# Kernel optimization log

Measured on AMD Instinct MI355X. Metric: run time of the kernel, lower is better.

Reference implementation:

```python
import jax, jax.numpy as jnp
import numpy as np

C = 256
G = 32            # GroupNorm groups = min(32, C)
DQK = C // 8      # q/k channel dim
EPS = 1e-5


def setup_inputs() -> dict:
    key = jax.random.key(0)
    ks = jax.random.split(key, 10)
    B, H, W = 4, 64, 64
    s = 0.02
    return {
        "x": jax.random.normal(ks[0], (B, C, H, W), dtype=jnp.float32),
        "gamma": jnp.ones((C,), jnp.float32),
        "beta": jnp.zeros((C,), jnp.float32),
        "wq": jax.random.normal(ks[1], (DQK, C), jnp.float32) * s,
        "bq": jnp.zeros((DQK,), jnp.float32),
        "wk": jax.random.normal(ks[2], (DQK, C), jnp.float32) * s,
        "bk": jnp.zeros((DQK,), jnp.float32),
        "wv": jax.random.normal(ks[3], (C, C), jnp.float32) * s,
        "bv": jnp.zeros((C,), jnp.float32),
        "wp": jax.random.normal(ks[4], (C, C), jnp.float32) * s,
        "bp": jnpp if False else jnp.zeros((C,), jnp.float32),
    }


def reference(x, gamma, beta, wq, bq, wk, bk, wv, bv, wp, bp):
    B, Cc, H, W = x.shape
    N = H * W
    # GroupNorm(32, C), affine
    h = x.reshape(B, G, Cc // G, H, W)
    mu = h.mean(axis=(2, 3, 4), keepdims=True)
    var = h.var(axis=(2, 3, 4), keepdims=True)
    h = (h - mu) * jax.lax.rsqrt(var + EPS)
    h = h.reshape(B, Cc, N) * gamma[:, None] + beta[:, None]
    # 1x1 convs == per-token linear maps over channels
    q = jnp.einsum('dc,bcn->bnd', wq, h) + bq            # [B, N, DQK]
    k = jnp.einsum('dc,bcn->bdn', wk, h) + bk[:, None]   # [B, DQK, N]
    v = jnp.einsum('ec,bcn->ben', wv, h) + bv[:, None]   # [B, C, N]
    scale = DQK ** (-0.5)
    attn = jax.nn.softmax(jnp.einsum('bnd,bdm->bnm', q, k) * scale, axis=-1)
    out = jnp.einsum('bnm,bem->ben', attn, v)            # [B, C, N]
    proj = jnp.einsum('fe,ben->bfn', wp, out) + bp[:, None]
    return x + proj.reshape(B, Cc, H, W)
```

## Files before the change

kernel.cpp:

```cpp
#include <hip/hip_runtime.h>
#include <hip/hip_bf16.h>

#define NB 4
#define CD 256
#define NT 4096
#define DQ 32

typedef __attribute__((ext_vector_type(8))) __bf16 bf16x8;
typedef __attribute__((ext_vector_type(16))) float float16v;
typedef __attribute__((ext_vector_type(4))) unsigned int uint4v;
typedef __attribute__((ext_vector_type(2))) unsigned int uint2v;

#if __has_builtin(__builtin_amdgcn_exp2f)
#define EXP2(x) __builtin_amdgcn_exp2f(x)
#else
#define EXP2(x) exp2f(x)
#endif

__device__ inline unsigned short f2bf(float f) {
  unsigned u = __float_as_uint(f);
  u += 0x7fffu + ((u >> 16) & 1u);
  return (unsigned short)(u >> 16);
}

#define BARRIER() asm volatile("s_waitcnt lgkmcnt(0)\n\ts_barrier" ::: "memory")

__global__ __launch_bounds__(1024) void stats_pack(
    const float* __restrict__ x, const float* __restrict__ gamma,
    const float* __restrict__ beta, const float* __restrict__ wq,
    const float* __restrict__ wk, const float* __restrict__ wv,
    const float* __restrict__ wp, const float* __restrict__ bq,
    const float* __restrict__ bk, const float* __restrict__ bv,
    float* __restrict__ sc, float* __restrict__ sh,
    unsigned short* __restrict__ wqkv, unsigned short* __restrict__ wpb,
    float* __restrict__ bias) {
  int bx = blockIdx.x;
  int tid = threadIdx.x;
  if (bx < 128) {
    int b = bx >> 5, g = bx & 31;
    const float4* xp = (const float4*)(x + (size_t)bx * 32768);
    float s = 0.f, ss = 0.f;
#pragma unroll
    for (int i = 0; i < 8; i++) {
      float4 t4 = xp[i * 1024 + tid];
      s += t4.x + t4.y + t4.z + t4.w;
      ss += t4.x * t4.x + t4.y * t4.y + t4.z * t4.z + t4.w * t4.w;
    }
#pragma unroll
    for (int off = 32; off >= 1; off >>= 1) {
      s += __shfl_xor(s, off);
      ss += __shfl_xor(ss, off);
    }
    __shared__ float red[32];
    int wid = tid >> 6;
    if ((tid & 63) == 0) {
      red[wid] = s;
      red[16 + wid] = ss;
    }
    __syncthreads();
    if (tid < 8) {
      float S = 0.f, SS = 0.f;
#pragma unroll
      for (int i = 0; i < 16; i++) {
        S += red[i];
        SS += red[16 + i];
      }
      float mu = S * (1.f / 32768.f);
      float rstd = rsqrtf(SS * (1.f / 32768.f) - mu * mu + 1e-5f);
      int c = g * 8 + tid;
      float gm = gamma[c];
      sc[b * CD + c] = gm * rstd;
      sh[b * CD + c] = beta[c] - mu * gm * rstd;
    }
  } else {
    const float scale2 = 0.2550348909867343f;
    int i = (bx - 128) * 1024 + tid;
    if (i < 320 * 256) {
      int j = i >> 8, c = i & 255;
      float v;
      if (j < 32) v = wq[j * 256 + c] * scale2;
      else if (j < 64) v = wk[(j - 32) * 256 + c];
      else v = wv[(j - 64) * 256 + c];
      wqkv[i] = f2bf(v);
    } else if (i < 320 * 256 + 256 * 256) {
      int k = i - 320 * 256;
      wpb[k] = f2bf(wp[k]);
    } else if (i < 320 * 256 + 256 * 256 + 320) {
      int j = i - (320 * 256 + 256 * 256);
      float v;
      if (j < 32) v = bq[j] * scale2;
      else if (j < 64) v = bk[j - 32];
      else v = bv[j - 64];
      bias[j] = v;
    }
  }
}

__global__ __launch_bounds__(512) void qkv_norm(
    const float* __restrict__ x, const float* __restrict__ sc,
    const float* __restrict__ sh, const unsigned short* __restrict__ A,
    const float* __restrict__ bias, unsigned short* __restrict__ qk,
    unsigned short* __restrict__ v) {
  int nt = blockIdx.x, b = blockIdx.y;
  int tid = threadIdx.x, lane = tid & 63, w = tid >> 6;
  int l31 = lane & 31, hh = lane >> 5;
  int n0 = nt * 64;

  __shared__ unsigned short Hs[64 * 262];
  const float* xb = x + (size_t)b * CD * NT + n0;
  const float* scb = sc + b * CD;
  const float* shb = sh + b * CD;
#pragma unroll
  for (int u = 0; u < 4; u++) {
    int c0 = (w + 8 * u) * 8;
    float4 s0 = *(const float4*)(scb + c0);
    float4 s1 = *(const float4*)(scb + c0 + 4);
    float4 h0 = *(const float4*)(shb + c0);
    float4 h1 = *(const float4*)(shb + c0 + 4);
    float scv[8] = {s0.x, s0.y, s0.z, s0.w, s1.x, s1.y, s1.z, s1.w};
    float shv[8] = {h0.x, h0.y, h0.z, h0.w, h1.x, h1.y, h1.z, h1.w};
    unsigned short hv[8];
#pragma unroll
    for (int j = 0; j < 8; j++) {
      float val = xb[(size_t)(c0 + j) * NT + lane];
      hv[j] = f2bf(val * scv[j] + shv[j]);
    }
    *(uint4v*)&Hs[lane * 262 + c0] = *(uint4v*)hv;
  }
  __syncthreads();

  if (w < 5) {
    int m_base = w * 64;
    const unsigned short* Ar0 = A + (size_t)(m_base + l31) * 256 + 8 * hh;
    const unsigned short* Ar1 = Ar0 + (size_t)32 * 256;
    const unsigned short* B0 = &Hs[l31 * 262 + 8 * hh];
    const unsigned short* B1 = &Hs[(32 + l31) * 262 + 8 * hh];
    float16v a00, a01, a10, a11;
#pragma unroll
    for (int r = 0; r < 16; r++) {
      a00[r] = 0.f; a01[r] = 0.f; a10[r] = 0.f; a11[r] = 0.f;
    }
#pragma unroll
    for (int s = 0; s < 16; s++) {
      bf16x8 af0 = *(const bf16x8*)(Ar0 + 16 * s);
      bf16x8 af1 = *(const bf16x8*)(Ar1 + 16 * s);
      bf16x8 bf0 = *(const bf16x8*)(B0 + 16 * s);
      bf16x8 bf1 = *(const bf16x8*)(B1 + 16 * s);
      a00 = __builtin_amdgcn_mfma_f32_32x32x16_bf16(af0, bf0, a00, 0, 0, 0);
      a01 = __builtin_amdgcn_mfma_f32_32x32x16_bf16(af0, bf1, a01, 0, 0, 0);
      a10 = __builtin_amdgcn_mfma_f32_32x32x16_bf16(af1, bf0, a10, 0, 0, 0);
      a11 = __builtin_amdgcn_mfma_f32_32x32x16_bf16(af1, bf1, a11, 0, 0, 0);
    }
#pragma unroll
    for (int mi = 0; mi < 2; mi++) {
#pragma unroll
      for (int nq = 0; nq < 2; nq++) {
        int n = n0 + nq * 32 + l31;
        int itg = n >> 6, sp = (n >> 4) & 3;
        int lsn = ((n >> 3) & 1) * 32;
        int el = n & 7;
#pragma unroll
        for (int r = 0; r < 16; r++) {
          int j = m_base + 32 * mi + (r & 3) + 8 * (r >> 2) + 4 * hh;
          float val = (mi ? (nq ? a11[r] : a10[r]) : (nq ? a01[r] : a00[r])) +
                      bias[j];
          if (j < 64) {
            qk[((size_t)b * NT + n) * 64 + j] = f2bf(val);
          } else {
            int e = j - 64;
            int et = e >> 5;
            v[((((size_t)b * 64 + itg) * 8 + et) * 4 + sp) * 512 +
              (lsn + (e & 31)) * 8 + el] = f2bf(val);
          }
        }
      }
    }
  }
}

#define K_STAGE2(TNEXT, KSW)                                                  \
  if (tid >= 256) {                                                           \
    *(uint4v*)&Ks[(KSW) * 2304 + skr * 36 + skc] = kregA;                     \
    *(uint4v*)&Ks[((KSW) + 1) * 2304 + skr * 36 + skc] = kregB;               \
    int ta_ = (TNEXT) > 31 ? 31 : (TNEXT);                                    \
    int tb_ = (TNEXT) + 1 > 31 ? 31 : (TNEXT) + 1;                            \
    kregA =                                                                   \
        *(const uint4v*)&qkb[(size_t)(mbase + ta_ * 64 + skr) * 64 + 32 + skc]; \
    kregB =                                                                   \
        *(const uint4v*)&qkb[(size_t)(mbase + tb_ * 64 + skr) * 64 + 32 + skc]; \
  }

#define QK_ONE(KSB, PBB)                                                      \
  if (w < 4) {                                                                \
    float16v st;                                                              \
    _Pragma("unroll") for (int r = 0; r < 16; r++) st[r] = 0.f;               \
    __builtin_amdgcn_s_setprio(1);                                            \
    _Pragma("unroll") for (int s = 0; s < 2; s++) {                           \
      bf16x8 af = *(const bf16x8*)&Ks[(KSB) * 2304 + (32 * ks2 + l31) * 36 +  \
                                      16 * s + 8 * hh];                       \
      st = __builtin_amdgcn_mfma_f32_32x32x16_bf16(af, qfr[s], st, 0, 0, 0);  \
    }                                                                         \
    __builtin_amdgcn_s_setprio(0);                                            \
    _Pragma("unroll") for (int rq = 0; rq < 4; rq++) {                        \
      float e0 = EXP2(st[4 * rq + 0]);                                        \
      float e1 = EXP2(st[4 * rq + 1]);                                        \
      float e2 = EXP2(st[4 * rq + 2]);                                        \
      float e3 = EXP2(st[4 * rq + 3]);                                        \
      lsum += (e0 + e1) + (e2 + e3);                                          \
      uint2v pw;                                                              \
      pw[0] = __builtin_amdgcn_perm(__float_as_uint(e1), __float_as_uint(e0), \
                                    0x07060302u);                             \
      pw[1] = __builtin_amdgcn_perm(__float_as_uint(e3), __float_as_uint(e2), \
                                    0x07060302u);                             \
      *(uint2v*)&Pbuf[(PBB) * 4352 + (qs * 32 + l31) * 68 + 8 * rq + 4 * hh + \
                      32 * ks2] = pw;                                         \
    }                                                                         \
  }

#define PV_ONE(PBB, VS)                                                       \
  {                                                                           \
    __builtin_amdgcn_s_setprio(1);                                            \
    _Pragma("unroll") for (int sp = 0; sp < 4; sp++) {                        \
      bf16x8 a0 =                                                             \
          *(const bf16x8*)&Pbuf[(PBB) * 4352 + l31 * 68 + 16 * sp + 8 * hh];  \
      bf16x8 a1 = *(const bf16x8*)&Pbuf[(PBB) * 4352 + (32 + l31) * 68 +      \
                                        16 * sp + 8 * hh];                    \
      acc[0] =                                                                \
          __builtin_amdgcn_mfma_f32_32x32x16_bf16(a0, VS[sp], acc[0], 0, 0, 0); \
      acc[1] =                                                                \
          __builtin_amdgcn_mfma_f32_32x32x16_bf16(a1, VS[sp], acc[1], 0, 0, 0); \
    }                                                                         \
    __builtin_amdgcn_s_setprio(0);                                            \
  }

#define V_LOAD2(T)                                                            \
  {                                                                           \
    const unsigned short* vp0_ = vbase + (size_t)(T)*16384;                   \
    const unsigned short* vp1_ = vbase + (size_t)((T) + 1) * 16384;           \
    _Pragma("unroll") for (int u = 0; u < 4; u++) {                           \
      vS0[u] = *(const bf16x8*)(vp0_ + u * 512);                              \
      vS1[u] = *(const bf16x8*)(vp1_ + u * 512);                              \
    }                                                                         \
  }

__global__ __launch_bounds__(512, 4) void attn_fused(
    const unsigned short* __restrict__ qk, const unsigned short* __restrict__ Vp,
    unsigned short* __restrict__ Pa, unsigned short* __restrict__ Pb,
    float* __restrict__ lp4) {
  int L = blockIdx.x;
  int xv = L & 7;
  int b = xv >> 1;
  int kh = xv & 1;
  int n0 = (L >> 3) * 64;
  int tid = threadIdx.x, lane = tid & 63, w = tid >> 6;
  int l31 = lane & 31, hh = lane >> 5;
  int qs = w & 1, ks2 = (w >> 1) & 1;

  __shared__ unsigned short Ks[4 * 2304];
  __shared__ unsigned short Pbuf[4 * 4352];

  const unsigned short* qkb = qk + (size_t)b * NT * 64;
  const unsigned short* vit = Vp + ((size_t)b * 64 + kh * 32) * 16384;
  const unsigned short* vbase = vit + (size_t)w * 4 * 512 + lane * 8;

  bf16x8 qfr[2];
  if (w < 4) {
    int n_g = n0 + 32 * qs + l31;
    qfr[0] = *(const bf16x8*)&qkb[(size_t)n_g * 64 + 8 * hh];
    qfr[1] = *(const bf16x8*)&qkb[(size_t)n_g * 64 + 8 * hh + 16];
  }

  int tK = tid - 256;
  int skr = tK >> 2, skc = (tK & 3) * 8;
  int mbase = kh * 2048;
  uint4v kregA, kregB;

  float16v acc[2];
#pragma unroll
  for (int q2 = 0; q2 < 2; q2++)
#pragma unroll
    for (int r = 0; r < 16; r++) acc[q2][r] = 0.f;
  float lsum = 0.f;

  bf16x8 vS0[4], vS1[4];
  if (tid >= 256) {
    kregA = *(const uint4v*)&qkb[(size_t)(mbase + skr) * 64 + 32 + skc];
    kregB = *(const uint4v*)&qkb[(size_t)(mbase + 64 + skr) * 64 + 32 + skc];
    *(uint4v*)&Ks[skr * 36 + skc] = kregA;
    *(uint4v*)&Ks[2304 + skr * 36 + skc] = kregB;
    kregA = *(const uint4v*)&qkb[(size_t)(mbase + 128 + skr) * 64 + 32 + skc];
    kregB = *(const uint4v*)&qkb[(size_t)(mbase + 192 + skr) * 64 + 32 + skc];
  }
  BARRIER();

  K_STAGE2(4, 2);
  QK_ONE(0, 0);
  QK_ONE(1, 1);
  V_LOAD2(0);
  BARRIER();

  for (int p = 1; p < 15; p += 2) {
    K_STAGE2(2 * p + 4, 0);
    QK_ONE(2, 2);
    QK_ONE(3, 3);
    PV_ONE(0, vS0);
    PV_ONE(1, vS1);
    V_LOAD2(2 * p);
    BARRIER();
    K_STAGE2(2 * p + 6, 2);
    QK_ONE(0, 0);
    QK_ONE(1, 1);
    PV_ONE(2, vS0);
    PV_ONE(3, vS1);
    V_LOAD2(2 * p + 2);
    BARRIER();
  }
  K_STAGE2(34, 0);
  QK_ONE(2, 2);
  QK_ONE(3, 3);
  PV_ONE(0, vS0);
  PV_ONE(1, vS1);
  V_LOAD2(30);
  BARRIER();
  PV_ONE(2, vS0);
  PV_ONE(3, vS1);

  if (w < 4) {
    lsum += __shfl_xor(lsum, 32);
    if (hh == 0) {
      lp4[(size_t)((kh * 2 + ks2) * NB + b) * NT + n0 + 32 * qs + l31] = lsum;
    }
  }

  unsigned short* Pout = (kh ? Pb : Pa) + (size_t)b * NT * CD;
#pragma unroll
  for (int r = 0; r < 16; r++) {
    int nl = (r & 3) + 8 * (r >> 2) + 4 * hh;
    Pout[(size_t)(n0 + nl) * CD + 32 * w + l31] = f2bf(acc[0][r]);
    Pout[(size_t)(n0 + 32 + nl) * CD + 32 * w + l31] = f2bf(acc[1][r]);
  }
}

__global__ __launch_bounds__(256) void proj_gemm(
    const unsigned short* __restrict__ Wp, const unsigned short* __restrict__ Pa,
    const unsigned short* __restrict__ Pb, const float* __restrict__ lp4,
    const float* __restrict__ bp, const float* __restrict__ x,
    float* __restrict__ out) {
  int nt = blockIdx.x, mh = blockIdx.y, b = blockIdx.z;
  int tid = threadIdx.x, lane = tid & 63;
  int w = tid >> 6;
  int l31 = lane & 31, hh = lane >> 5;
  int n0 = nt * 64;

  __shared__ unsigned short Bs[64 * 260];
  int r0 = tid >> 5, colb = (tid & 31) * 8;
#pragma unroll
  for (int u = 0; u < 8; u++) {
    int row = r0 + 8 * u;
    float lA = 0.f;
#pragma unroll
    for (int s4 = 0; s4 < 4; s4++)
      lA += lp4[(size_t)(s4 * NB + b) * NT + n0 + row];
    float inv = 1.f / lA;
    size_t goff = ((size_t)b * NT + n0 + row) * CD + colb;
    uint4v ua = *(const uint4v*)(Pa + goff);
    uint4v ub = *(const uint4v*)(Pb + goff);
    uint4v rr;
#pragma unroll
    for (int j = 0; j < 4; j++) {
      float lo = __uint_as_float(ua[j] << 16) + __uint_as_float(ub[j] << 16);
      float hi = __uint_as_float(ua[j] & 0xffff0000u) +
                 __uint_as_float(ub[j] & 0xffff0000u);
      lo *= inv;
      hi *= inv;
      rr[j] = __builtin_amdgcn_perm(__float_as_uint(hi), __float_as_uint(lo),
                                    0x07060302u);
    }
    *(uint4v*)&Bs[row * 260 + colb] = rr;
  }
  __syncthreads();

  int m_base = mh * 128 + w * 32;
  const unsigned short* Arow = Wp + (size_t)(m_base + l31) * 256 + 8 * hh;
  const unsigned short* b0p = &Bs[l31 * 260 + 8 * hh];
  const unsigned short* b1p = &Bs[(32 + l31) * 260 + 8 * hh];
  float16v acc0, acc1;
#pragma unroll
  for (int r = 0; r < 16; r++) { acc0[r] = 0.f; acc1[r] = 0.f; }
#pragma unroll
  for (int s = 0; s < 16; s++) {
    bf16x8 af = *(const bf16x8*)(Arow + 16 * s);
    bf16x8 bf0 = *(const bf16x8*)(b0p + 16 * s);
    bf16x8 bf1 = *(const bf16x8*)(b1p + 16 * s);
    acc0 = __builtin_amdgcn_mfma_f32_32x32x16_bf16(af, bf0, acc0, 0, 0, 0);
    acc1 = __builtin_amdgcn_mfma_f32_32x32x16_bf16(af, bf1, acc1, 0, 0, 0);
  }
#pragma unroll
  for (int nq = 0; nq < 2; nq++) {
    int n = n0 + nq * 32 + l31;
#pragma unroll
    for (int r = 0; r < 16; r++) {
      int f = m_base + (r & 3) + 8 * (r >> 2) + 4 * hh;
      size_t idx = ((size_t)b * CD + f) * NT + n;
      out[idx] = x[idx] + (nq ? acc1[r] : acc0[r]) + bp[f];
    }
  }
}

extern "C" void kernel_launch(void* const* d_in, const int* in_sizes, int n_in,
                              void* d_out, int out_size, void* d_ws,
                              size_t ws_size, hipStream_t stream) {
  (void)in_sizes; (void)n_in; (void)out_size; (void)ws_size;
  const float* x = (const float*)d_in[0];
  const float* gamma = (const float*)d_in[1];
  const float* beta = (const float*)d_in[2];
  const float* wq = (const float*)d_in[3];
  const float* bq = (const float*)d_in[4];
  const float* wk = (const float*)d_in[5];
  const float* bk = (const float*)d_in[6];
  const float* wv = (const float*)d_in[7];
  const float* bv = (const float*)d_in[8];
  const float* wp = (const float*)d_in[9];
  const float* bp = (const float*)d_in[10];
  float* out = (float*)d_out;

  char* ws = (char*)d_ws;
  unsigned short* pa_ws = (unsigned short*)ws;
  unsigned short* qk_ws = (unsigned short*)(ws + 8388608);
  unsigned short* v_ws = (unsigned short*)(ws + 10485760);
  unsigned short* o_ws = (unsigned short*)(ws + 18874368);
  unsigned short* wqkv_b = (unsigned short*)(ws + 27262976);
  unsigned short* wp_b = (unsigned short*)(ws + 27426816);
  float* bias_q = (float*)(ws + 27557888);
  float* lp4 = (float*)(ws + 27563264);
  float* sc_ws = (float*)(ws + 27825408);
  float* sh_ws = (float*)(ws + 27829504);

  stats_pack<<<273, 1024, 0, stream>>>(x, gamma, beta, wq, wk, wv, wp, bq, bk,
                                       bv, sc_ws, sh_ws, wqkv_b, wp_b, bias_q);
  dim3 gq(64, NB);
  qkv_norm<<<gq, 512, 0, stream>>>(x, sc_ws, sh_ws, wqkv_b, bias_q, qk_ws,
                                   v_ws);
  attn_fused<<<512, 512, 0, stream>>>(qk_ws, v_ws, pa_ws, o_ws, lp4);
  dim3 gp(64, 2, NB);
  proj_gemm<<<gp, 256, 0, stream>>>(wp_b, pa_ws, o_ws, lp4, bp, x, out);
}
```

Before: 174.8 us.

## Split QK/softmax and K staging evenly across all eight waves

Work in the fused attention kernel is redistributed. Before, waves 0-3 computed both QK tiles per step and waves 4-7 staged K. Now every wave computes one QK tile (selected by its wave half) and every thread stages one K row chunk. The row-sum partials grow from four to eight slices, so the projection kernel sums eight partials and the workspace offsets shift. The aim is to remove the load imbalance in which half the waves sat idle during the exp/softmax phase, at the cost of extra partial-sum traffic.

```diff
diff --git a/kernel.cpp b/kernel.cpp
--- a/kernel.cpp
+++ b/kernel.cpp
@@ -178,25 +178,22 @@
   }
 }
 
-#define K_STAGE2(TNEXT, KSW)                                                  \
-  if (tid >= 256) {                                                           \
-    *(uint4v*)&Ks[(KSW) * 2304 + skr * 36 + skc] = kregA;                     \
-    *(uint4v*)&Ks[((KSW) + 1) * 2304 + skr * 36 + skc] = kregB;               \
-    int ta_ = (TNEXT) > 31 ? 31 : (TNEXT);                                    \
-    int tb_ = (TNEXT) + 1 > 31 ? 31 : (TNEXT) + 1;                            \
-    kregA =                                                                   \
-        *(const uint4v*)&qkb[(size_t)(mbase + ta_ * 64 + skr) * 64 + 32 + skc]; \
-    kregB =                                                                   \
-        *(const uint4v*)&qkb[(size_t)(mbase + tb_ * 64 + skr) * 64 + 32 + skc]; \
-  }
-
-#define QK_ONE(KSB, PBB)                                                      \
-  if (w < 4) {                                                                \
+#define K_STAGE2R(TNEXT)                                                      \
+  {                                                                           \
+    *(uint4v*)&Ks[((((TNEXT)-2) + ksel) & 3) * 2304 + skr * 36 + skc] = kreg; \
+    int tt_ = (TNEXT) + ksel;                                                 \
+    if (tt_ > 31) tt_ = 31;                                                   \
+    kreg = *(const uint4v*)&qkb[(size_t)(mbase + tt_ * 64 + skr) * 64 + 32 +  \
+                                skc];                                         \
+  }
+
+#define QK_ONE(QB)                                                            \
+  {                                                                           \
     float16v st;                                                              \
     _Pragma("unroll") for (int r = 0; r < 16; r++) st[r] = 0.f;               \
     __builtin_amdgcn_s_setprio(1);                                            \
     _Pragma("unroll") for (int s = 0; s < 2; s++) {                           \
-      bf16x8 af = *(const bf16x8*)&Ks[(KSB) * 2304 + (32 * ks2 + l31) * 36 +  \
+      bf16x8 af = *(const bf16x8*)&Ks[(QB) * 2304 + (32 * ks2 + l31) * 36 +   \
                                       16 * s + 8 * hh];                       \
       st = __builtin_amdgcn_mfma_f32_32x32x16_bf16(af, qfr[s], st, 0, 0, 0);  \
     }                                                                         \
@@ -212,7 +209,7 @@
                                     0x07060302u);                             \
       pw[1] = __builtin_amdgcn_perm(__float_as_uint(e3), __float_as_uint(e2), \
                                     0x07060302u);                             \
-      *(uint2v*)&Pbuf[(PBB) * 4352 + (qs * 32 + l31) * 68 + 8 * rq + 4 * hh + \
+      *(uint2v*)&Pbuf[(QB) * 4352 + (qs * 32 + l31) * 68 + 8 * rq + 4 * hh +  \
                       32 * ks2] = pw;                                         \
     }                                                                         \
   }
@@ -246,7 +243,7 @@
 __global__ __launch_bounds__(512, 4) void attn_fused(
     const unsigned short* __restrict__ qk, const unsigned short* __restrict__ Vp,
     unsigned short* __restrict__ Pa, unsigned short* __restrict__ Pb,
-    float* __restrict__ lp4) {
+    float* __restrict__ lp8) {
   int L = blockIdx.x;
   int xv = L & 7;
   int b = xv >> 1;
@@ -254,6 +251,7 @@
   int n0 = (L >> 3) * 64;
   int tid = threadIdx.x, lane = tid & 63, w = tid >> 6;
   int l31 = lane & 31, hh = lane >> 5;
+  int tp = w >> 2;
   int qs = w & 1, ks2 = (w >> 1) & 1;
 
   __shared__ unsigned short Ks[4 * 2304];
@@ -264,16 +262,16 @@
   const unsigned short* vbase = vit + (size_t)w * 4 * 512 + lane * 8;
 
   bf16x8 qfr[2];
-  if (w < 4) {
+  {
     int n_g = n0 + 32 * qs + l31;
     qfr[0] = *(const bf16x8*)&qkb[(size_t)n_g * 64 + 8 * hh];
     qfr[1] = *(const bf16x8*)&qkb[(size_t)n_g * 64 + 8 * hh + 16];
   }
 
-  int tK = tid - 256;
-  int skr = tK >> 2, skc = (tK & 3) * 8;
+  int ksel = tid >> 8;
+  int skr = (tid & 255) >> 2, skc = (tid & 3) * 8;
   int mbase = kh * 2048;
-  uint4v kregA, kregB;
+  uint4v kreg;
 
   float16v acc[2];
 #pragma unroll
@@ -283,41 +281,32 @@
   float lsum = 0.f;
 
   bf16x8 vS0[4], vS1[4];
-  if (tid >= 256) {
-    kregA = *(const uint4v*)&qkb[(size_t)(mbase + skr) * 64 + 32 + skc];
-    kregB = *(const uint4v*)&qkb[(size_t)(mbase + 64 + skr) * 64 + 32 + skc];
-    *(uint4v*)&Ks[skr * 36 + skc] = kregA;
-    *(uint4v*)&Ks[2304 + skr * 36 + skc] = kregB;
-    kregA = *(const uint4v*)&qkb[(size_t)(mbase + 128 + skr) * 64 + 32 + skc];
-    kregB = *(const uint4v*)&qkb[(size_t)(mbase + 192 + skr) * 64 + 32 + skc];
-  }
+  kreg = *(const uint4v*)&qkb[(size_t)(mbase + ksel * 64 + skr) * 64 + 32 + skc];
+  *(uint4v*)&Ks[ksel * 2304 + skr * 36 + skc] = kreg;
+  kreg = *(const uint4v*)&qkb[(size_t)(mbase + (2 + ksel) * 64 + skr) * 64 +
+                              32 + skc];
   BARRIER();
 
-  K_STAGE2(4, 2);
-  QK_ONE(0, 0);
-  QK_ONE(1, 1);
+  K_STAGE2R(4);
+  QK_ONE(tp);
   V_LOAD2(0);
   BARRIER();
 
   for (int p = 1; p < 15; p += 2) {
-    K_STAGE2(2 * p + 4, 0);
-    QK_ONE(2, 2);
-    QK_ONE(3, 3);
+    K_STAGE2R(2 * p + 4);
+    QK_ONE(2 + tp);
     PV_ONE(0, vS0);
     PV_ONE(1, vS1);
     V_LOAD2(2 * p);
     BARRIER();
-    K_STAGE2(2 * p + 6, 2);
-    QK_ONE(0, 0);
-    QK_ONE(1, 1);
+    K_STAGE2R(2 * p + 6);
+    QK_ONE(tp);
     PV_ONE(2, vS0);
     PV_ONE(3, vS1);
     V_LOAD2(2 * p + 2);
     BARRIER();
   }
-  K_STAGE2(34, 0);
-  QK_ONE(2, 2);
-  QK_ONE(3, 3);
+  QK_ONE(2 + tp);
   PV_ONE(0, vS0);
   PV_ONE(1, vS1);
   V_LOAD2(30);
@@ -325,11 +314,10 @@
   PV_ONE(2, vS0);
   PV_ONE(3, vS1);
 
-  if (w < 4) {
-    lsum += __shfl_xor(lsum, 32);
-    if (hh == 0) {
-      lp4[(size_t)((kh * 2 + ks2) * NB + b) * NT + n0 + 32 * qs + l31] = lsum;
-    }
+  lsum += __shfl_xor(lsum, 32);
+  if (hh == 0) {
+    lp8[(size_t)((kh * 4 + tp * 2 + ks2) * NB + b) * NT + n0 + 32 * qs + l31] =
+        lsum;
   }
 
   unsigned short* Pout = (kh ? Pb : Pa) + (size_t)b * NT * CD;
@@ -343,7 +331,7 @@
 
 __global__ __launch_bounds__(256) void proj_gemm(
     const unsigned short* __restrict__ Wp, const unsigned short* __restrict__ Pa,
-    const unsigned short* __restrict__ Pb, const float* __restrict__ lp4,
+    const unsigned short* __restrict__ Pb, const float* __restrict__ lp8,
     const float* __restrict__ bp, const float* __restrict__ x,
     float* __restrict__ out) {
   int nt = blockIdx.x, mh = blockIdx.y, b = blockIdx.z;
@@ -359,8 +347,8 @@
     int row = r0 + 8 * u;
     float lA = 0.f;
 #pragma unroll
-    for (int s4 = 0; s4 < 4; s4++)
-      lA += lp4[(size_t)(s4 * NB + b) * NT + n0 + row];
+    for (int s4 = 0; s4 < 8; s4++)
+      lA += lp8[(size_t)(s4 * NB + b) * NT + n0 + row];
     float inv = 1.f / lA;
     size_t goff = ((size_t)b * NT + n0 + row) * CD + colb;
     uint4v ua = *(const uint4v*)(Pa + goff);
@@ -432,16 +420,16 @@
   unsigned short* wqkv_b = (unsigned short*)(ws + 27262976);
   unsigned short* wp_b = (unsigned short*)(ws + 27426816);
   float* bias_q = (float*)(ws + 27557888);
-  float* lp4 = (float*)(ws + 27563264);
-  float* sc_ws = (float*)(ws + 27825408);
-  float* sh_ws = (float*)(ws + 27829504);
+  float* lp8 = (float*)(ws + 27563264);
+  float* sc_ws = (float*)(ws + 28087552);
+  float* sh_ws = (float*)(ws + 28091648);
 
   stats_pack<<<273, 1024, 0, stream>>>(x, gamma, beta, wq, wk, wv, wp, bq, bk,
                                        bv, sc_ws, sh_ws, wqkv_b, wp_b, bias_q);
   dim3 gq(64, NB);
   qkv_norm<<<gq, 512, 0, stream>>>(x, sc_ws, sh_ws, wqkv_b, bias_q, qk_ws,
                                    v_ws);
-  attn_fused<<<512, 512, 0, stream>>>(qk_ws, v_ws, pa_ws, o_ws, lp4);
+  attn_fused<<<512, 512, 0, stream>>>(qk_ws, v_ws, pa_ws, o_ws, lp8);
   dim3 gp(64, 2, NB);
-  proj_gemm<<<gp, 256, 0, stream>>>(wp_b, pa_ws, o_ws, lp4, bp, x, out);
-}
+  proj_gemm<<<gp, 256, 0, stream>>>(wp_b, pa_ws, o_ws, lp8, bp, x, out);
+}
```

After: 177.2 us. No clear change (+1.4%).
